# Kernel tuning notes

Hardware: AMD Instinct MI355X
Metric: run time of the kernel (lower is better)

## Reference

```python
import jax, jax.numpy as jnp
import numpy as np

N_NODES = 10000   # graph_size1 == graph_size2 (coarse graph nodes)
AS1 = 8           # arr_size1 (input block size)
AS2 = 8           # arr_size2 (output block size)
E = 320000        # number of coarse edges
B = 32            # batch
SIZE1 = N_NODES * AS1
SIZE2 = N_NODES * AS2


def setup_inputs() -> dict:
    key = jax.random.key(0)
    k1, k2, k3, k4 = jax.random.split(key, 4)
    x = jax.random.normal(k1, (B, SIZE1, 1), dtype=jnp.float32)
    indices = jax.random.randint(k2, (2, E), 0, N_NODES, dtype=jnp.int32)
    # torch init: uniform_(0,1) on values (the second uniform_ overwrote the first)
    values = jax.random.uniform(k3, (E, AS1, AS2), dtype=jnp.float32)  # v[e,i,j]
    inv = 1.0 / (E * AS1 * AS2)
    b = jax.random.uniform(k4, (SIZE2,), dtype=jnp.float32, minval=-inv, maxval=inv)
    return {"x": x, "values": values, "b": b, "indices": indices}


def reference(x, values, b, indices):
    # Expanded sparse entry: A[t0*AS2 + j, t1*AS1 + i] = values[e, i, j]
    # => out_block[t0, j] += sum_i values[e,i,j] * x_block[t1, i]
    rows = indices[0]  # output coarse node per edge
    cols = indices[1]  # input coarse node per edge
    xb = x.reshape(B, N_NODES, AS1)          # view input as coarse blocks
    xg = xb[:, cols, :]                      # (B, E, AS1) irregular gather
    contrib = jnp.einsum('bei,eij->bej', xg, values)  # (B, E, AS2)
    out = jax.ops.segment_sum(contrib.transpose(1, 0, 2), rows,
                              num_segments=N_NODES)   # (N_NODES, B, AS2)
    out = out.transpose(1, 0, 2).reshape(B, SIZE2, 1)
    return out + b[None, :, None]
```

## Files before the change

kernel.cpp:

```cpp
#include <hip/hip_runtime.h>
#include <stddef.h>

#define N_NODES 10000
#define NE 320000
#define NB 32
#define SIZE1 80000
#define SIZE2 80000

#define WS_PAIRS   0
#define WS_COUNTS  640000
#define WS_OFFSETS 650000
#define WS_CURSOR  660002
#define WS_BSUMS   670016
#define WS_XT      680000

typedef short short8 __attribute__((ext_vector_type(8)));
typedef float floatx4 __attribute__((ext_vector_type(4)));
union FragU { short8 v; ushort us[8]; uint4 u4; };

__device__ inline ushort f2bf(float f) {
  union { float f; unsigned u; } c; c.f = f;
  unsigned u = c.u;
  u += 0x7fffu + ((u >> 16) & 1u);
  return (ushort)(u >> 16);
}

__global__ __launch_bounds__(256) void prep_kernel(const float* __restrict__ x,
                                                   ushort* __restrict__ xt,
                                                   const int* __restrict__ idxs,
                                                   int* __restrict__ counts) {
  {
    int e = blockIdx.x * 256 + threadIdx.x;
    if (e < NE) atomicAdd(&counts[idxs[e]], 1);
  }
  if (blockIdx.x >= 313) return;
  __shared__ float s[32 * 260];
  const int t = threadIdx.x;
  const int n0 = blockIdx.x * 32;
#pragma unroll
  for (int it = 0; it < 8; ++it) {
    int idx = it * 256 + t;
    int b = idx >> 6, q = idx & 63;
    int base = n0 * 8 + q * 4;
    float4 v = make_float4(0.f, 0.f, 0.f, 0.f);
    if (base < SIZE1) v = *(const float4*)&x[(size_t)b * SIZE1 + base];
    *(float4*)&s[b * 260 + q * 4] = v;
  }
  __syncthreads();
#pragma unroll
  for (int r = 0; r < 4; ++r) {
    int p = r * 256 + t;
    int nl = p >> 5, b = p & 31;
    int n = n0 + nl;
    if (n < N_NODES) {
      FragU f;
      const float* row = &s[b * 260 + nl * 8];
#pragma unroll
      for (int i = 0; i < 8; ++i) f.us[i] = f2bf(row[i]);
      *(uint4*)&xt[(size_t)n * 256 + b * 8] = f.u4;
    }
  }
}

__global__ __launch_bounds__(256) void scanA_kernel(const int* __restrict__ counts,
                                                    int* __restrict__ offsets,
                                                    int* __restrict__ bsums) {
  __shared__ int s[256];
  const int t = threadIdx.x;
  const int i = blockIdx.x * 256 + t;
  int c = (i < N_NODES) ? counts[i] : 0;
  s[t] = c;
  __syncthreads();
#pragma unroll
  for (int d = 1; d < 256; d <<= 1) {
    int v = (t >= d) ? s[t - d] : 0;
    __syncthreads();
    s[t] += v;
    __syncthreads();
  }
  if (i < N_NODES) offsets[i] = s[t] - c;
  if (t == 255) bsums[blockIdx.x] = s[255];
}

__global__ __launch_bounds__(256) void scanC_kernel(int* __restrict__ offsets,
                                                    int* __restrict__ cursor,
                                                    const int* __restrict__ bsums) {
  const int t = threadIdx.x;
  const int nb = blockIdx.x;
  const int i = nb * 256 + t;
  int p = 0;
  for (int w = 0; w < nb; ++w) p += bsums[w];
  if (i < N_NODES) {
    int v = offsets[i] + p;
    offsets[i] = v;
    cursor[i] = v;
  }
  if (i == 0) offsets[N_NODES] = NE;
}

__global__ __launch_bounds__(256) void scatter_kernel(const int* __restrict__ idxs,
                                                      int* __restrict__ cursor,
                                                      int2* __restrict__ pairs) {
  int e = blockIdx.x * 256 + threadIdx.x;
  if (e < NE) {
    int r = idxs[e];
    int c = idxs[NE + e];
    int pos = atomicAdd(&cursor[r], 1);
    pairs[pos] = make_int2(c, e);
  }
}

__global__ __launch_bounds__(256) void gather_mfma_kernel(const ushort* __restrict__ xt,
                                                          const float* __restrict__ vals,
                                                          const float* __restrict__ bias,
                                                          const int* __restrict__ offsets,
                                                          const int2* __restrict__ pairs,
                                                          float* __restrict__ out) {
  __shared__ float red[3][64][9];
  const int t = threadIdx.x;
  const int lane = t & 63;
  const int w = t >> 6;
  const int n = blockIdx.x;
  const int quad = lane >> 4;
  const int nn = lane & 15;
  const int beg = offsets[n];
  const int end = offsets[n + 1];

  floatx4 acc0 = {0.f, 0.f, 0.f, 0.f};
  floatx4 acc1 = {0.f, 0.f, 0.f, 0.f};

  for (int base = beg; base < end; base += 64) {
    const int lim = min(64, end - base);
    int2 pv = pairs[min(base + lane, end - 1)];
    const int nslots = (lim + 3) >> 2;

    for (int s0 = w; s0 < nslots; s0 += 8) {
      FragU alo0, ahi0, b0, alo1, ahi1, b1;
      {
        const int le = s0 * 4 + quad;
        const int lec = min(le, lim - 1);
        const int px = __shfl(pv.x, lec);
        const int pe = __shfl(pv.y, lec);
        const bool valid = le < lim;
        const ushort* xr = xt + (size_t)px * 256;
        alo0.u4 = *(const uint4*)(xr + nn * 8);
        ahi0.u4 = *(const uint4*)(xr + (16 + nn) * 8);
        b0.u4 = make_uint4(0, 0, 0, 0);
        if (nn < 8 && valid) {
          const float* vp = vals + (size_t)pe * 64 + nn;
#pragma unroll
          for (int v = 0; v < 8; ++v) b0.us[v] = f2bf(vp[v * 8]);
        }
      }
      {
        const int le = (s0 + 4) * 4 + quad;
        const int lec = min(le, lim - 1);
        const int px = __shfl(pv.x, lec);
        const int pe = __shfl(pv.y, lec);
        const bool valid = le < lim;
        const ushort* xr = xt + (size_t)px * 256;
        alo1.u4 = *(const uint4*)(xr + nn * 8);
        ahi1.u4 = *(const uint4*)(xr + (16 + nn) * 8);
        b1.u4 = make_uint4(0, 0, 0, 0);
        if (nn < 8 && valid) {
          const float* vp = vals + (size_t)pe * 64 + nn;
#pragma unroll
          for (int v = 0; v < 8; ++v) b1.us[v] = f2bf(vp[v * 8]);
        }
      }
      acc0 = __builtin_amdgcn_mfma_f32_16x16x32_bf16(alo0.v, b0.v, acc0, 0, 0, 0);
      acc1 = __builtin_amdgcn_mfma_f32_16x16x32_bf16(ahi0.v, b0.v, acc1, 0, 0, 0);
      acc0 = __builtin_amdgcn_mfma_f32_16x16x32_bf16(alo1.v, b1.v, acc0, 0, 0, 0);
      acc1 = __builtin_amdgcn_mfma_f32_16x16x32_bf16(ahi1.v, b1.v, acc1, 0, 0, 0);
    }
  }

  if (w > 0) {
#pragma unroll
    for (int r = 0; r < 4; ++r) {
      red[w - 1][lane][r] = acc0[r];
      red[w - 1][lane][4 + r] = acc1[r];
    }
  }
  __syncthreads();
  if (w == 0) {
#pragma unroll
    for (int j = 0; j < 3; ++j)
#pragma unroll
      for (int r = 0; r < 4; ++r) {
        acc0[r] += red[j][lane][r];
        acc1[r] += red[j][lane][4 + r];
      }
    if (nn < 8) {
      float bz = bias[n * 8 + nn];
#pragma unroll
      for (int r = 0; r < 4; ++r) {
        out[(size_t)(quad * 4 + r) * SIZE2 + n * 8 + nn] = acc0[r] + bz;
        out[(size_t)(16 + quad * 4 + r) * SIZE2 + n * 8 + nn] = acc1[r] + bz;
      }
    }
  }
}

extern "C" void kernel_launch(void* const* d_in, const int* in_sizes, int n_in,
                              void* d_out, int out_size, void* d_ws, size_t ws_size,
                              hipStream_t stream) {
  const float* x    = (const float*)d_in[0];
  const float* vals = (const float*)d_in[1];
  const float* bias = (const float*)d_in[2];
  const int*   idxs = (const int*)d_in[3];
  float* out = (float*)d_out;

  int* ws = (int*)d_ws;
  int2* pairs    = (int2*)(ws + WS_PAIRS);
  int* counts    = ws + WS_COUNTS;
  int* offsets   = ws + WS_OFFSETS;
  int* cursor    = ws + WS_CURSOR;
  int* bsums     = ws + WS_BSUMS;
  ushort* xt     = (ushort*)(ws + WS_XT);

  hipMemsetAsync(counts, 0, N_NODES * sizeof(int), stream);

  const int egrid = (NE + 255) / 256;
  const int ngrid = (N_NODES + 255) / 256;
  prep_kernel<<<egrid, 256, 0, stream>>>(x, xt, idxs, counts);
  scanA_kernel<<<ngrid, 256, 0, stream>>>(counts, offsets, bsums);
  scanC_kernel<<<ngrid, 256, 0, stream>>>(offsets, cursor, bsums);
  scatter_kernel<<<egrid, 256, 0, stream>>>(idxs, cursor, pairs);
  gather_mfma_kernel<<<N_NODES, 256, 0, stream>>>(xt, vals, bias, offsets, pairs, out);
}
```

Baseline: 201.2 us.

## Pre-convert edge values to bf16 in CSR order during scatter

The scatter kernel now converts each edge's 8x8 value block to bf16 and writes it, already in MFMA fragment layout, to a CSR-ordered buffer. Only column indices are stored in place of (col, edge) pairs. The gather kernel then loads B fragments with one contiguous 16-byte read instead of eight strided float loads plus conversions from randomly ordered edges. The cost is an extra pass that writes about 41MB of bf16 values, which adds a scattered write stream in the scatter kernel. The bounds check on the edge index in scatter is removed, which is safe only because NE divides evenly by 256.

```diff
diff --git a/kernel.cpp b/kernel.cpp
--- a/kernel.cpp
+++ b/kernel.cpp
@@ -7,12 +7,13 @@
 #define SIZE1 80000
 #define SIZE2 80000
 
-#define WS_PAIRS   0
-#define WS_COUNTS  640000
-#define WS_OFFSETS 650000
-#define WS_CURSOR  660002
-#define WS_BSUMS   670016
-#define WS_XT      680000
+#define WS_COLS    0
+#define WS_COUNTS  320000
+#define WS_OFFSETS 330000
+#define WS_CURSOR  340002
+#define WS_BSUMS   350016
+#define WS_XT      350080
+#define WS_VCSR    1630080
 
 typedef short short8 __attribute__((ext_vector_type(8)));
 typedef float floatx4 __attribute__((ext_vector_type(4)));
@@ -98,23 +99,39 @@
   if (i == 0) offsets[N_NODES] = NE;
 }
 
-__global__ __launch_bounds__(256) void scatter_kernel(const int* __restrict__ idxs,
+__global__ __launch_bounds__(256) void scatter_kernel(const float* __restrict__ vals,
+                                                      const int* __restrict__ idxs,
                                                       int* __restrict__ cursor,
-                                                      int2* __restrict__ pairs) {
-  int e = blockIdx.x * 256 + threadIdx.x;
-  if (e < NE) {
-    int r = idxs[e];
-    int c = idxs[NE + e];
-    int pos = atomicAdd(&cursor[r], 1);
-    pairs[pos] = make_int2(c, e);
+                                                      int* __restrict__ cols_csr,
+                                                      ushort* __restrict__ vcsr) {
+  const int t = threadIdx.x;
+  const int lane = t & 63;
+  const int e = blockIdx.x * 256 + t;
+  const int r = idxs[e];
+  const int c = idxs[NE + e];
+  const int pos = atomicAdd(&cursor[r], 1);
+  cols_csr[pos] = c;
+
+  const int ebase = e - lane;
+  const int kk = lane >> 3;
+  const int j = lane & 7;
+#pragma unroll
+  for (int it = 0; it < 8; ++it) {
+    const int k = it * 8 + kk;
+    const int pk = __shfl(pos, k);
+    const float* vp = vals + (size_t)(ebase + k) * 64 + j;
+    FragU f;
+#pragma unroll
+    for (int i = 0; i < 8; ++i) f.us[i] = f2bf(vp[i * 8]);
+    *(uint4*)(vcsr + (size_t)pk * 64 + j * 8) = f.u4;
   }
 }
 
 __global__ __launch_bounds__(256) void gather_mfma_kernel(const ushort* __restrict__ xt,
-                                                          const float* __restrict__ vals,
+                                                          const ushort* __restrict__ vcsr,
                                                           const float* __restrict__ bias,
                                                           const int* __restrict__ offsets,
-                                                          const int2* __restrict__ pairs,
+                                                          const int* __restrict__ cols_csr,
                                                           float* __restrict__ out) {
   __shared__ float red[3][64][9];
   const int t = threadIdx.x;
@@ -131,7 +148,7 @@
 
   for (int base = beg; base < end; base += 64) {
     const int lim = min(64, end - base);
-    int2 pv = pairs[min(base + lane, end - 1)];
+    int cv = cols_csr[min(base + lane, end - 1)];
     const int nslots = (lim + 3) >> 2;
 
     for (int s0 = w; s0 < nslots; s0 += 8) {
@@ -139,34 +156,26 @@
       {
         const int le = s0 * 4 + quad;
         const int lec = min(le, lim - 1);
-        const int px = __shfl(pv.x, lec);
-        const int pe = __shfl(pv.y, lec);
+        const int px = __shfl(cv, lec);
         const bool valid = le < lim;
         const ushort* xr = xt + (size_t)px * 256;
         alo0.u4 = *(const uint4*)(xr + nn * 8);
         ahi0.u4 = *(const uint4*)(xr + (16 + nn) * 8);
         b0.u4 = make_uint4(0, 0, 0, 0);
-        if (nn < 8 && valid) {
-          const float* vp = vals + (size_t)pe * 64 + nn;
-#pragma unroll
-          for (int v = 0; v < 8; ++v) b0.us[v] = f2bf(vp[v * 8]);
-        }
+        if (nn < 8 && valid)
+          b0.u4 = *(const uint4*)(vcsr + (size_t)(base + le) * 64 + nn * 8);
       }
       {
         const int le = (s0 + 4) * 4 + quad;
         const int lec = min(le, lim - 1);
-        const int px = __shfl(pv.x, lec);
-        const int pe = __shfl(pv.y, lec);
+        const int px = __shfl(cv, lec);
         const bool valid = le < lim;
         const ushort* xr = xt + (size_t)px * 256;
         alo1.u4 = *(const uint4*)(xr + nn * 8);
         ahi1.u4 = *(const uint4*)(xr + (16 + nn) * 8);
         b1.u4 = make_uint4(0, 0, 0, 0);
-        if (nn < 8 && valid) {
-          const float* vp = vals + (size_t)pe * 64 + nn;
-#pragma unroll
-          for (int v = 0; v < 8; ++v) b1.us[v] = f2bf(vp[v * 8]);
-        }
+        if (nn < 8 && valid)
+          b1.u4 = *(const uint4*)(vcsr + (size_t)(base + le) * 64 + nn * 8);
       }
       acc0 = __builtin_amdgcn_mfma_f32_16x16x32_bf16(alo0.v, b0.v, acc0, 0, 0, 0);
       acc1 = __builtin_amdgcn_mfma_f32_16x16x32_bf16(ahi0.v, b0.v, acc1, 0, 0, 0);
@@ -212,12 +221,13 @@
   float* out = (float*)d_out;
 
   int* ws = (int*)d_ws;
-  int2* pairs    = (int2*)(ws + WS_PAIRS);
+  int* cols_csr  = ws + WS_COLS;
   int* counts    = ws + WS_COUNTS;
   int* offsets   = ws + WS_OFFSETS;
   int* cursor    = ws + WS_CURSOR;
   int* bsums     = ws + WS_BSUMS;
   ushort* xt     = (ushort*)(ws + WS_XT);
+  ushort* vcsr   = (ushort*)(ws + WS_VCSR);
 
   hipMemsetAsync(counts, 0, N_NODES * sizeof(int), stream);
 
@@ -226,6 +236,6 @@
   prep_kernel<<<egrid, 256, 0, stream>>>(x, xt, idxs, counts);
   scanA_kernel<<<ngrid, 256, 0, stream>>>(counts, offsets, bsums);
   scanC_kernel<<<ngrid, 256, 0, stream>>>(offsets, cursor, bsums);
-  scatter_kernel<<<egrid, 256, 0, stream>>>(idxs, cursor, pairs);
-  gather_mfma_kernel<<<N_NODES, 256, 0, stream>>>(xt, vals, bias, offsets, pairs, out);
-}
+  scatter_kernel<<<egrid, 256, 0, stream>>>(vals, idxs, cursor, cols_csr, vcsr);
+  gather_mfma_kernel<<<N_NODES, 256, 0, stream>>>(xt, vcsr, bias, offsets, cols_csr, out);
+}
```

Measured after the change: 199.8 us. Within noise of the previous version (-0.7%).
